# Optimization experiments

Measured on AMD Instinct MI355X. Metric: run time of the kernel, lower is better.

## Reference

```python
import jax, jax.numpy as jnp
import numpy as np

N_NODES = 50000
N_EDGES = 800000
IN_DIM = 128
NUM_GRAPHS = 64
NEG_SLOPE = 0.2  # PyG GATConv default


def _gat_layer(x, src, dst, W, a_s, a_d, b):
    """PyG GATConv (concat=True), eval mode (no dropout).
    x: [N, Fin]; W: [H*C, Fin]; a_s, a_d: [H, C]; b: [H*C]."""
    N = x.shape[0]
    H, C = a_s.shape
    h = (x @ W.T).reshape(N, H, C)                      # [N,H,C]
    es = jnp.einsum('nhc,hc->nh', h, a_s)               # [N,H]
    ed = jnp.einsum('nhc,hc->nh', h, a_d)               # [N,H]
    e = jax.nn.leaky_relu(es[src] + ed[dst], NEG_SLOPE)  # [E,H]
    # segment softmax over incoming edges of each destination node
    m = jax.ops.segment_max(e, dst, num_segments=N)     # [N,H]
    ex = jnp.exp(e - m[dst])
    denom = jax.ops.segment_sum(ex, dst, num_segments=N)
    alpha = ex / denom[dst]                             # [E,H]
    out = jax.ops.segment_sum(h[src] * alpha[:, :, None], dst, num_segments=N)
    return out.reshape(N, H * C) + b


def _make_params(key):
    dims = [(512, IN_DIM, 8, 64), (256, 512, 8, 32), (128, 256, 8, 16), (512, 128, 8, 64)]
    ps = {}
    k = key
    for i, (out_f, in_f, H, C) in enumerate(dims, 1):
        k, k1, k2, k3 = jax.random.split(k, 4)
        s = 1.0 / np.sqrt(in_f)
        ps[f'W{i}'] = jax.random.normal(k1, (out_f, in_f), jnp.float32) * s
        ps[f'a{i}s'] = jax.random.normal(k2, (H, C), jnp.float32) * 0.1
        ps[f'a{i}d'] = jax.random.normal(k3, (H, C), jnp.float32) * 0.1
        ps[f'b{i}'] = jnp.zeros((out_f,), jnp.float32)
    k, k1, k2 = jax.random.split(k, 3)
    ps['lw1'] = jax.random.normal(k1, (32, 512), jnp.float32) * (1.0 / np.sqrt(512))
    ps['lb1'] = jnp.zeros((32,), jnp.float32)
    ps['lw2'] = jax.random.normal(k2, (2, 32), jnp.float32) * (1.0 / np.sqrt(32))
    ps['lb2'] = jnp.zeros((2,), jnp.float32)
    return ps


def setup_inputs() -> dict:
    key = jax.random.key(0)
    kx, ke, kb, kp = jax.random.split(key, 4)
    x = jax.random.normal(kx, (N_NODES, IN_DIM), jnp.float32)
    edge_index = jax.random.randint(ke, (2, N_EDGES), 0, N_NODES, jnp.int64 if jax.config.jax_enable_x64 else jnp.int32)
    batch = jnp.sort(jax.random.randint(kb, (N_NODES,), 0, NUM_GRAPHS, edge_index.dtype))
    inp = {'x': x, 'edge_index': edge_index, 'batch': batch}
    inp.update(_make_params(kp))
    return inp


def reference(x, edge_index, batch,
              W1, a1s, a1d, b1, W2, a2s, a2d, b2,
              W3, a3s, a3d, b3, W4, a4s, a4d, b4,
              lw1, lb1, lw2, lb2):
    N = x.shape[0]
    # PyG GATConv add_self_loops=True
    loop = jnp.arange(N, dtype=edge_index.dtype)
    src = jnp.concatenate([edge_index[0], loop])
    dst = jnp.concatenate([edge_index[1], loop])

    h = jax.nn.elu(_gat_layer(x, src, dst, W1, a1s, a1d, b1))
    h = jax.nn.elu(_gat_layer(h, src, dst, W2, a2s, a2d, b2))
    h = jax.nn.elu(_gat_layer(h, src, dst, W3, a3s, a3d, b3))
    h = _gat_layer(h, src, dst, W4, a4s, a4d, b4)

    # global mean pool over graphs
    sums = jax.ops.segment_sum(h, batch, num_segments=NUM_GRAPHS)
    cnts = jax.ops.segment_sum(jnp.ones((N, 1), h.dtype), batch, num_segments=NUM_GRAPHS)
    g = sums / jnp.maximum(cnts, 1.0)                   # [G, 512]

    g = jax.nn.elu(g @ lw1.T + lb1)                     # dropout skipped (eval)
    return g @ lw2.T + lb2                              # [G, 2]
```

## Files before the change

kernel.cpp:

```cpp
#include <hip/hip_runtime.h>
#include <math.h>

#define NN 50000
#define NE 800000
#define NEP (NE + NN)
#define NGR 64
#define NHEAD 8
#define MPAD 50048

typedef short short8 __attribute__((ext_vector_type(8)));
typedef float floatx4 __attribute__((ext_vector_type(4)));
typedef unsigned uintx4 __attribute__((ext_vector_type(4)));

__device__ inline float bf2f(short s) {
    union { unsigned u; float f; } v;
    v.u = ((unsigned)(unsigned short)s) << 16;
    return v.f;
}
__device__ inline float bf2f_lo(unsigned p) {
    union { unsigned u; float f; } v; v.u = p << 16; return v.f;
}
__device__ inline float bf2f_hi(unsigned p) {
    union { unsigned u; float f; } v; v.u = p & 0xffff0000u; return v.f;
}
__device__ inline short f2bf(float f) {
    union { float f; unsigned u; } v; v.f = f;
    unsigned r = v.u + 0x7fffu + ((v.u >> 16) & 1u);
    return (short)(r >> 16);
}

__global__ void count_deg(const int* __restrict__ ei, int* __restrict__ deg) {
    int e = blockIdx.x * 256 + threadIdx.x;
    if (e >= NEP) return;
    int d = (e < NE) ? ei[NE + e] : (e - NE);
    atomicAdd(&deg[d], 1);
}

__global__ __launch_bounds__(1024) void scan_local(const int* __restrict__ deg,
                                                   int* __restrict__ out,
                                                   int* __restrict__ bsum, int n) {
    __shared__ int sd[1024];
    int b = blockIdx.x, t = threadIdx.x;
    int i = b * 1024 + t;
    int v = (i < n) ? deg[i] : 0;
    sd[t] = v;
    __syncthreads();
    for (int off = 1; off < 1024; off <<= 1) {
        int tmp = (t >= off) ? sd[t - off] : 0;
        __syncthreads();
        sd[t] += tmp;
        __syncthreads();
    }
    if (i < n) out[i] = sd[t] - v;
    if (t == 1023) bsum[b] = sd[1023];
}

__global__ void scan_bsum(int* __restrict__ bsum, int nb) {
    if (threadIdx.x == 0) {
        int s = 0;
        for (int i = 0; i < nb; i++) { int v = bsum[i]; bsum[i] = s; s += v; }
        bsum[nb] = s;
    }
}

__global__ void scan_add(int* __restrict__ row_ptr, int* __restrict__ cursor,
                         const int* __restrict__ bsum, int n, int nb) {
    int i = blockIdx.x * 256 + threadIdx.x;
    if (i < n) {
        int v = row_ptr[i] + bsum[i >> 10];
        row_ptr[i] = v;
        cursor[i] = v;
    } else if (i == n) {
        row_ptr[n] = bsum[nb];
    }
}

__global__ void scatter_edges(const int* __restrict__ ei, int* __restrict__ cursor,
                              int* __restrict__ srcs) {
    int e = blockIdx.x * 256 + threadIdx.x;
    if (e >= NEP) return;
    int s, d;
    if (e < NE) { s = ei[e]; d = ei[NE + e]; }
    else        { s = e - NE; d = e - NE; }
    int pos = atomicAdd(&cursor[d], 1);
    srcs[pos] = s;
}

__global__ void conv_f2bf(const float* __restrict__ in, short* __restrict__ out, int n) {
    int i = blockIdx.x * 256 + threadIdx.x;
    if (i < n) out[i] = f2bf(in[i]);
}

__global__ void conv_x_pad4(const float* __restrict__ x, short* __restrict__ xb) {
    int i = blockIdx.x * 256 + threadIdx.x;
    if (i >= MPAD * 32) return;
    int r = i >> 5;
    short4 o;
    if (r < NN) {
        float4 v = *(const float4*)&x[(size_t)i * 4];
        o.x = f2bf(v.x); o.y = f2bf(v.y); o.z = f2bf(v.z); o.w = f2bf(v.w);
    } else {
        o.x = o.y = o.z = o.w = 0;
    }
    *(short4*)&xb[(size_t)i * 4] = o;
}

#define LDA 40
__global__ __launch_bounds__(256) void gemm_bf(const short* __restrict__ A,
                                               const short* __restrict__ B,
                                               short* __restrict__ C,
                                               int K, int Nc, int colTiles) {
    __shared__ __align__(16) short As[128 * LDA];
    __shared__ __align__(16) short Bs[128 * LDA];
    int bx = blockIdx.x % colTiles;
    int by = blockIdx.x / colTiles;
    int row0 = by * 128, col0 = bx * 128;
    int t = threadIdx.x;
    int lane = t & 63, w = t >> 6;
    int wr = (w >> 1) * 64, wc = (w & 1) * 64;
    int lrow = lane & 15, lq = lane >> 4;

    floatx4 acc[4][4];
#pragma unroll
    for (int i = 0; i < 4; i++)
#pragma unroll
        for (int j = 0; j < 4; j++) acc[i][j] = (floatx4)0.0f;

    for (int k0 = 0; k0 < K; k0 += 32) {
#pragma unroll
        for (int i = 0; i < 2; i++) {
            int chunk = t + i * 256;
            int r = chunk >> 2;
            int kc = (chunk & 3) * 8;
            *(short8*)&As[r * LDA + kc] = *(const short8*)&A[(size_t)(row0 + r) * K + k0 + kc];
            *(short8*)&Bs[r * LDA + kc] = *(const short8*)&B[(size_t)(col0 + r) * K + k0 + kc];
        }
        __syncthreads();
        short8 af[4], bfr[4];
#pragma unroll
        for (int i = 0; i < 4; i++)
            af[i] = *(const short8*)&As[(wr + i * 16 + lrow) * LDA + lq * 8];
#pragma unroll
        for (int j = 0; j < 4; j++)
            bfr[j] = *(const short8*)&Bs[(wc + j * 16 + lrow) * LDA + lq * 8];
#pragma unroll
        for (int i = 0; i < 4; i++)
#pragma unroll
            for (int j = 0; j < 4; j++)
                acc[i][j] = __builtin_amdgcn_mfma_f32_16x16x32_bf16(af[i], bfr[j], acc[i][j], 0, 0, 0);
        __syncthreads();
    }
#pragma unroll
    for (int i = 0; i < 4; i++)
#pragma unroll
        for (int j = 0; j < 4; j++)
#pragma unroll
            for (int r = 0; r < 4; r++) {
                int row = row0 + wr + i * 16 + lq * 4 + r;
                int col = col0 + wc + j * 16 + lrow;
                C[(size_t)row * Nc + col] = f2bf(acc[i][j][r]);
            }
}

template <int C>
__global__ void compute_esed(const short* __restrict__ h, const float* __restrict__ a_s,
                             const float* __restrict__ a_d, float* __restrict__ es,
                             float* __restrict__ ed) {
    int gid = blockIdx.x * 256 + threadIdx.x;
    if (gid >= NN * NHEAD) return;
    int n = gid >> 3, hh = gid & 7;
    const short* hr = h + (size_t)n * NHEAD * C + hh * C;
    const float* as = a_s + hh * C;
    const float* ad = a_d + hh * C;
    float s1 = 0.f, s2 = 0.f;
#pragma unroll
    for (int c = 0; c < C; c += 8) {
        short8 hv = *(const short8*)&hr[c];
#pragma unroll
        for (int j = 0; j < 8; j++) {
            float hvf = bf2f(hv[j]);
            s1 = fmaf(hvf, as[c + j], s1);
            s2 = fmaf(hvf, ad[c + j], s2);
        }
    }
    es[gid] = s1;
    ed[gid] = s2;
}

template <int C, bool ELU>
__global__ __launch_bounds__(256) void attn_wave(const short* __restrict__ h,
                                                 const float* __restrict__ es,
                                                 const float* __restrict__ ed,
                                                 const int* __restrict__ row_ptr,
                                                 const int* __restrict__ srcs,
                                                 const float* __restrict__ bias,
                                                 short* __restrict__ out) {
    constexpr int HC = NHEAD * C;
    constexpr int TPR = HC / 8;
    constexpr int EPI = 64 / TPR;
    int wave = threadIdx.x >> 6, lane = threadIdx.x & 63;
    int n = blockIdx.x * 4 + wave;
    int start = row_ptr[n];
    int deg = row_ptr[n + 1] - start;
    int hh1 = lane & 7;
    float edv = ed[n * 8 + hh1];

    float pm = -1e30f;
    for (int idx = lane; idx < deg * 8; idx += 64) {
        int s = srcs[start + (idx >> 3)];
        float e = es[s * 8 + hh1] + edv;
        e = e > 0.f ? e : 0.2f * e;
        pm = fmaxf(pm, e);
    }
    pm = fmaxf(pm, __shfl_xor(pm, 8));
    pm = fmaxf(pm, __shfl_xor(pm, 16));
    pm = fmaxf(pm, __shfl_xor(pm, 32));

    float ps = 0.f;
    for (int idx = lane; idx < deg * 8; idx += 64) {
        int s = srcs[start + (idx >> 3)];
        float e = es[s * 8 + hh1] + edv;
        e = e > 0.f ? e : 0.2f * e;
        ps += __expf(e - pm);
    }
    ps += __shfl_xor(ps, 8);
    ps += __shfl_xor(ps, 16);
    ps += __shfl_xor(ps, 32);
    float invd = 1.0f / ps;

    int sub = lane & (TPR - 1);
    int c0 = sub * 8;
    int hh = c0 / C;
    float mh3 = __shfl(pm, hh);
    float iv3 = __shfl(invd, hh);
    float ed3 = __shfl(edv, hh);

    float acc[8];
#pragma unroll
    for (int j = 0; j < 8; j++) acc[j] = 0.f;

    for (int k = lane / TPR; k < deg; k += EPI) {
        int s = srcs[start + k];
        float e = es[s * 8 + hh] + ed3;
        e = e > 0.f ? e : 0.2f * e;
        float wv = __expf(e - mh3) * iv3;
        uintx4 hv = *(const uintx4*)&h[(size_t)s * HC + c0];
#pragma unroll
        for (int j = 0; j < 4; j++) {
            acc[2 * j]     = fmaf(wv, bf2f_lo(hv[j]), acc[2 * j]);
            acc[2 * j + 1] = fmaf(wv, bf2f_hi(hv[j]), acc[2 * j + 1]);
        }
    }
    if (EPI >= 2) {
#pragma unroll
        for (int j = 0; j < 8; j++) acc[j] += __shfl_xor(acc[j], 32);
    }
    if (EPI == 4) {
#pragma unroll
        for (int j = 0; j < 8; j++) acc[j] += __shfl_xor(acc[j], 16);
    }
    if (lane < TPR) {
        floatx4 b0 = *(const floatx4*)&bias[c0];
        floatx4 b1 = *(const floatx4*)&bias[c0 + 4];
        float bb[8] = {b0[0], b0[1], b0[2], b0[3], b1[0], b1[1], b1[2], b1[3]};
        unsigned pk[4];
#pragma unroll
        for (int j = 0; j < 4; j++) {
            float o0 = acc[2 * j] + bb[2 * j];
            float o1 = acc[2 * j + 1] + bb[2 * j + 1];
            if (ELU) {
                o0 = o0 > 0.f ? o0 : (__expf(o0) - 1.0f);
                o1 = o1 > 0.f ? o1 : (__expf(o1) - 1.0f);
            }
            pk[j] = ((unsigned)(unsigned short)f2bf(o0)) |
                    (((unsigned)(unsigned short)f2bf(o1)) << 16);
        }
        *(uintx4*)&out[(size_t)n * HC + c0] = *(uintx4*)pk;
    }
}

__global__ __launch_bounds__(256) void pool_kernel(const short* __restrict__ h,
                                                   const int* __restrict__ batch,
                                                   float* __restrict__ gout) {
    __shared__ float red[256];
    int g = blockIdx.x >> 3;
    int fc = (blockIdx.x & 7) * 64;
    int lo = 0, hi = NN;
    while (lo < hi) { int mid = (lo + hi) >> 1; if (batch[mid] < g) lo = mid + 1; else hi = mid; }
    int s = lo;
    lo = 0; hi = NN;
    while (lo < hi) { int mid = (lo + hi) >> 1; if (batch[mid] < g + 1) lo = mid + 1; else hi = mid; }
    int e = lo;
    int t = threadIdx.x;
    int f = t & 63, stripe = t >> 6;
    float a = 0.f;
    for (int r = s + stripe; r < e; r += 4)
        a += bf2f(h[(size_t)r * 512 + fc + f]);
    red[t] = a;
    __syncthreads();
    if (t < 128) red[t] += red[t + 128];
    __syncthreads();
    if (t < 64) {
        float inv = 1.0f / fmaxf((float)(e - s), 1.0f);
        gout[g * 512 + fc + t] = (red[t] + red[t + 64]) * inv;
    }
}

__global__ __launch_bounds__(64) void mlp_kernel(const float* __restrict__ g,
                                                 const float* __restrict__ lw1,
                                                 const float* __restrict__ lb1,
                                                 const float* __restrict__ lw2,
                                                 const float* __restrict__ lb2,
                                                 float* __restrict__ outp) {
    __shared__ float gv[512];
    __shared__ float y1[32];
    int b = blockIdx.x, t = threadIdx.x;
    for (int i = t; i < 512; i += 64) gv[i] = g[b * 512 + i];
    __syncthreads();
    if (t < 32) {
        float a = lb1[t];
        for (int k = 0; k < 512; k++) a = fmaf(gv[k], lw1[t * 512 + k], a);
        y1[t] = a > 0.f ? a : (__expf(a) - 1.0f);
    }
    __syncthreads();
    if (t < 2) {
        float a = lb2[t];
        for (int k = 0; k < 32; k++) a = fmaf(y1[k], lw2[t * 32 + k], a);
        outp[b * 2 + t] = a;
    }
}

extern "C" void kernel_launch(void* const* d_in, const int* in_sizes, int n_in,
                              void* d_out, int out_size, void* d_ws, size_t ws_size,
                              hipStream_t stream) {
    (void)in_sizes; (void)n_in; (void)out_size; (void)ws_size;
    const float* x     = (const float*)d_in[0];
    const int*   ei    = (const int*)d_in[1];
    const int*   batch = (const int*)d_in[2];
    const float* W[4]  = {(const float*)d_in[3], (const float*)d_in[7],
                          (const float*)d_in[11], (const float*)d_in[15]};
    const float* As_[4] = {(const float*)d_in[4], (const float*)d_in[8],
                           (const float*)d_in[12], (const float*)d_in[16]};
    const float* Ad_[4] = {(const float*)d_in[5], (const float*)d_in[9],
                           (const float*)d_in[13], (const float*)d_in[17]};
    const float* Bi[4]  = {(const float*)d_in[6], (const float*)d_in[10],
                           (const float*)d_in[14], (const float*)d_in[18]};
    const float* lw1 = (const float*)d_in[19];
    const float* lb1 = (const float*)d_in[20];
    const float* lw2 = (const float*)d_in[21];
    const float* lb2 = (const float*)d_in[22];
    float* out = (float*)d_out;

    short* Ab = (short*)d_ws;
    short* Hb = Ab + (size_t)MPAD * 512;
    short* Wb = Hb + (size_t)MPAD * 512;
    short* Wb_[4] = {Wb, Wb + 65536, Wb + 196608, Wb + 229376};
    const int wsz[4] = {65536, 131072, 32768, 65536};
    float* esb  = (float*)(Wb + 294912);
    float* edb  = esb + NN * NHEAD;
    float* gbuf = edb + NN * NHEAD;
    int* row_ptr = (int*)(gbuf + NGR * 512);
    int* cursor  = row_ptr + (NN + 1);
    int* srcs    = cursor + (NN + 1);
    int* bsum    = srcs + NEP;

    const int nblk = (NN + 1023) / 1024;

    hipMemsetAsync(cursor, 0, NN * sizeof(int), stream);
    count_deg<<<(NEP + 255) / 256, 256, 0, stream>>>(ei, cursor);
    scan_local<<<nblk, 1024, 0, stream>>>(cursor, row_ptr, bsum, NN);
    scan_bsum<<<1, 64, 0, stream>>>(bsum, nblk);
    scan_add<<<(NN + 256) / 256, 256, 0, stream>>>(row_ptr, cursor, bsum, NN, nblk);
    scatter_edges<<<(NEP + 255) / 256, 256, 0, stream>>>(ei, cursor, srcs);

    conv_x_pad4<<<(MPAD * 32 + 255) / 256, 256, 0, stream>>>(x, Ab);
    for (int i = 0; i < 4; i++)
        conv_f2bf<<<(wsz[i] + 255) / 256, 256, 0, stream>>>(W[i], Wb_[i], wsz[i]);

    const int rowTiles = MPAD / 128;
    int eg = (NN * NHEAD + 255) / 256;
    const int ag = NN / 4;

    gemm_bf<<<rowTiles * 4, 256, 0, stream>>>(Ab, Wb_[0], Hb, 128, 512, 4);
    compute_esed<64><<<eg, 256, 0, stream>>>(Hb, As_[0], Ad_[0], esb, edb);
    attn_wave<64, true><<<ag, 256, 0, stream>>>(Hb, esb, edb, row_ptr, srcs, Bi[0], Ab);

    gemm_bf<<<rowTiles * 2, 256, 0, stream>>>(Ab, Wb_[1], Hb, 512, 256, 2);
    compute_esed<32><<<eg, 256, 0, stream>>>(Hb, As_[1], Ad_[1], esb, edb);
    attn_wave<32, true><<<ag, 256, 0, stream>>>(Hb, esb, edb, row_ptr, srcs, Bi[1], Ab);

    gemm_bf<<<rowTiles * 1, 256, 0, stream>>>(Ab, Wb_[2], Hb, 256, 128, 1);
    compute_esed<16><<<eg, 256, 0, stream>>>(Hb, As_[2], Ad_[2], esb, edb);
    attn_wave<16, true><<<ag, 256, 0, stream>>>(Hb, esb, edb, row_ptr, srcs, Bi[2], Ab);

    gemm_bf<<<rowTiles * 4, 256, 0, stream>>>(Ab, Wb_[3], Hb, 128, 512, 4);
    compute_esed<64><<<eg, 256, 0, stream>>>(Hb, As_[3], Ad_[3], esb, edb);
    attn_wave<64, false><<<ag, 256, 0, stream>>>(Hb, esb, edb, row_ptr, srcs, Bi[3], Ab);

    pool_kernel<<<NGR * 8, 256, 0, stream>>>(Ab, batch, gbuf);
    mlp_kernel<<<NGR, 64, 0, stream>>>(gbuf, lw1, lb1, lw2, lb2, out);
}
```

Measured before the change: 924.4 us.

## Fuse attention-score projection into GEMM epilogue and deepen K tile to 64

Removes the separate compute_esed kernel. The per-head es/ed dot products are now computed in the GEMM epilogue from the fp32 accumulators, using shuffle reductions across the 16 lanes that hold each row. This avoids re-reading the bf16 h matrix and saves one launch per layer. The GEMM K-step also grows from 32 to 64 (LDA 72), halving barrier count per tile at the cost of more shared memory. The scores are now computed from unrounded fp32 values instead of bf16 h, which slightly changes numerics.

```diff
diff --git a/kernel.cpp b/kernel.cpp
--- a/kernel.cpp
+++ b/kernel.cpp
@@ -105,11 +105,20 @@
     *(short4*)&xb[(size_t)i * 4] = o;
 }
 
-#define LDA 40
+#define LDA 72
+template <int C>
 __global__ __launch_bounds__(256) void gemm_bf(const short* __restrict__ A,
                                                const short* __restrict__ B,
-                                               short* __restrict__ C,
-                                               int K, int Nc, int colTiles) {
+                                               short* __restrict__ Cout,
+                                               const float* __restrict__ a_s,
+                                               const float* __restrict__ a_d,
+                                               float* __restrict__ es,
+                                               float* __restrict__ ed,
+                                               int K) {
+    constexpr int Nc = 8 * C;
+    constexpr int colTiles = Nc / 128;
+    constexpr int JPH = C / 16;
+    constexpr int HPW = 64 / C;
     __shared__ __align__(16) short As[128 * LDA];
     __shared__ __align__(16) short Bs[128 * LDA];
     int bx = blockIdx.x % colTiles;
@@ -126,30 +135,34 @@
 #pragma unroll
         for (int j = 0; j < 4; j++) acc[i][j] = (floatx4)0.0f;
 
-    for (int k0 = 0; k0 < K; k0 += 32) {
-#pragma unroll
-        for (int i = 0; i < 2; i++) {
+    for (int k0 = 0; k0 < K; k0 += 64) {
+#pragma unroll
+        for (int i = 0; i < 4; i++) {
             int chunk = t + i * 256;
-            int r = chunk >> 2;
-            int kc = (chunk & 3) * 8;
+            int r = chunk >> 3;
+            int kc = (chunk & 7) * 8;
             *(short8*)&As[r * LDA + kc] = *(const short8*)&A[(size_t)(row0 + r) * K + k0 + kc];
             *(short8*)&Bs[r * LDA + kc] = *(const short8*)&B[(size_t)(col0 + r) * K + k0 + kc];
         }
         __syncthreads();
-        short8 af[4], bfr[4];
-#pragma unroll
-        for (int i = 0; i < 4; i++)
-            af[i] = *(const short8*)&As[(wr + i * 16 + lrow) * LDA + lq * 8];
-#pragma unroll
-        for (int j = 0; j < 4; j++)
-            bfr[j] = *(const short8*)&Bs[(wc + j * 16 + lrow) * LDA + lq * 8];
-#pragma unroll
-        for (int i = 0; i < 4; i++)
+#pragma unroll
+        for (int kk = 0; kk < 2; kk++) {
+            short8 af[4], bfr[4];
+#pragma unroll
+            for (int i = 0; i < 4; i++)
+                af[i] = *(const short8*)&As[(wr + i * 16 + lrow) * LDA + kk * 32 + lq * 8];
 #pragma unroll
             for (int j = 0; j < 4; j++)
-                acc[i][j] = __builtin_amdgcn_mfma_f32_16x16x32_bf16(af[i], bfr[j], acc[i][j], 0, 0, 0);
+                bfr[j] = *(const short8*)&Bs[(wc + j * 16 + lrow) * LDA + kk * 32 + lq * 8];
+#pragma unroll
+            for (int i = 0; i < 4; i++)
+#pragma unroll
+                for (int j = 0; j < 4; j++)
+                    acc[i][j] = __builtin_amdgcn_mfma_f32_16x16x32_bf16(af[i], bfr[j], acc[i][j], 0, 0, 0);
+        }
         __syncthreads();
     }
+
 #pragma unroll
     for (int i = 0; i < 4; i++)
 #pragma unroll
@@ -158,33 +171,48 @@
             for (int r = 0; r < 4; r++) {
                 int row = row0 + wr + i * 16 + lq * 4 + r;
                 int col = col0 + wc + j * 16 + lrow;
-                C[(size_t)row * Nc + col] = f2bf(acc[i][j][r]);
+                Cout[(size_t)row * Nc + col] = f2bf(acc[i][j][r]);
             }
-}
-
-template <int C>
-__global__ void compute_esed(const short* __restrict__ h, const float* __restrict__ a_s,
-                             const float* __restrict__ a_d, float* __restrict__ es,
-                             float* __restrict__ ed) {
-    int gid = blockIdx.x * 256 + threadIdx.x;
-    if (gid >= NN * NHEAD) return;
-    int n = gid >> 3, hh = gid & 7;
-    const short* hr = h + (size_t)n * NHEAD * C + hh * C;
-    const float* as = a_s + hh * C;
-    const float* ad = a_d + hh * C;
-    float s1 = 0.f, s2 = 0.f;
-#pragma unroll
-    for (int c = 0; c < C; c += 8) {
-        short8 hv = *(const short8*)&hr[c];
-#pragma unroll
-        for (int j = 0; j < 8; j++) {
-            float hvf = bf2f(hv[j]);
-            s1 = fmaf(hvf, as[c + j], s1);
-            s2 = fmaf(hvf, ad[c + j], s2);
+
+    float asv[4], adv[4];
+#pragma unroll
+    for (int j = 0; j < 4; j++) {
+        int colA = col0 + wc + j * 16 + lrow;
+        asv[j] = a_s[colA];
+        adv[j] = a_d[colA];
+    }
+    int hb = (col0 + wc) / C;
+#pragma unroll
+    for (int i = 0; i < 4; i++)
+#pragma unroll
+        for (int r = 0; r < 4; r++) {
+            float s_h[HPW], d_h[HPW];
+#pragma unroll
+            for (int hh = 0; hh < HPW; hh++) { s_h[hh] = 0.f; d_h[hh] = 0.f; }
+#pragma unroll
+            for (int j = 0; j < 4; j++) {
+                s_h[j / JPH] = fmaf(acc[i][j][r], asv[j], s_h[j / JPH]);
+                d_h[j / JPH] = fmaf(acc[i][j][r], adv[j], d_h[j / JPH]);
+            }
+#pragma unroll
+            for (int hh = 0; hh < HPW; hh++) {
+#pragma unroll
+                for (int off = 1; off <= 8; off <<= 1) {
+                    s_h[hh] += __shfl_xor(s_h[hh], off);
+                    d_h[hh] += __shfl_xor(d_h[hh], off);
+                }
+            }
+            if (lrow == 0) {
+                int row = row0 + wr + i * 16 + lq * 4 + r;
+                if (row < NN) {
+#pragma unroll
+                    for (int hh = 0; hh < HPW; hh++) {
+                        es[row * 8 + hb + hh] = s_h[hh];
+                        ed[row * 8 + hb + hh] = d_h[hh];
+                    }
+                }
+            }
         }
-    }
-    es[gid] = s1;
-    ed[gid] = s2;
 }
 
 template <int C, bool ELU>
@@ -378,23 +406,18 @@
         conv_f2bf<<<(wsz[i] + 255) / 256, 256, 0, stream>>>(W[i], Wb_[i], wsz[i]);
 
     const int rowTiles = MPAD / 128;
-    int eg = (NN * NHEAD + 255) / 256;
     const int ag = NN / 4;
 
-    gemm_bf<<<rowTiles * 4, 256, 0, stream>>>(Ab, Wb_[0], Hb, 128, 512, 4);
-    compute_esed<64><<<eg, 256, 0, stream>>>(Hb, As_[0], Ad_[0], esb, edb);
+    gemm_bf<64><<<rowTiles * 4, 256, 0, stream>>>(Ab, Wb_[0], Hb, As_[0], Ad_[0], esb, edb, 128);
     attn_wave<64, true><<<ag, 256, 0, stream>>>(Hb, esb, edb, row_ptr, srcs, Bi[0], Ab);
 
-    gemm_bf<<<rowTiles * 2, 256, 0, stream>>>(Ab, Wb_[1], Hb, 512, 256, 2);
-    compute_esed<32><<<eg, 256, 0, stream>>>(Hb, As_[1], Ad_[1], esb, edb);
+    gemm_bf<32><<<rowTiles * 2, 256, 0, stream>>>(Ab, Wb_[1], Hb, As_[1], Ad_[1], esb, edb, 512);
     attn_wave<32, true><<<ag, 256, 0, stream>>>(Hb, esb, edb, row_ptr, srcs, Bi[1], Ab);
 
-    gemm_bf<<<rowTiles * 1, 256, 0, stream>>>(Ab, Wb_[2], Hb, 256, 128, 1);
-    compute_esed<16><<<eg, 256, 0, stream>>>(Hb, As_[2], Ad_[2], esb, edb);
+    gemm_bf<16><<<rowTiles * 1, 256, 0, stream>>>(Ab, Wb_[2], Hb, As_[2], Ad_[2], esb, edb, 256);
     attn_wave<16, true><<<ag, 256, 0, stream>>>(Hb, esb, edb, row_ptr, srcs, Bi[2], Ab);
 
-    gemm_bf<<<rowTiles * 4, 256, 0, stream>>>(Ab, Wb_[3], Hb, 128, 512, 4);
-    compute_esed<64><<<eg, 256, 0, stream>>>(Hb, As_[3], Ad_[3], esb, edb);
+    gemm_bf<64><<<rowTiles * 4, 256, 0, stream>>>(Ab, Wb_[3], Hb, As_[3], Ad_[3], esb, edb, 128);
     attn_wave<64, false><<<ag, 256, 0, stream>>>(Hb, esb, edb, row_ptr, srcs, Bi[3], Ab);
 
     pool_kernel<<<NGR * 8, 256, 0, stream>>>(Ab, batch, gbuf);
```

New measurement: 878.4 us. 5.0% less time.
